# Kernel tuning notes

Hardware: AMD Instinct MI355X
Metric: run time of the kernel (lower is better)

The kernel has to match this reference:

```python
import jax, jax.numpy as jnp
import numpy as np

B, T, S, D, V = 8, 128, 256, 512, 32000
NEG_INF = -1e9


def setup_inputs() -> dict:
    key = jax.random.key(0)
    ks = jax.random.split(key, 10)
    sc = 1.0 / np.sqrt(D)
    return {
        "logits": jax.random.normal(ks[0], (B, T, D), jnp.float32),
        "encoded_text": jax.random.normal(ks[1], (B, S, D), jnp.float32),
        "encoded_tgt": jax.random.normal(ks[2], (B, T, D), jnp.float32),
        "text": jax.random.randint(ks[3], (B, S), 0, V),
        "text_mask": jnp.ones((B, 1, S), dtype=bool),
        "vocab_gen": jax.random.normal(ks[4], (V, D), jnp.float32) * sc,
        "Wq": jax.random.normal(ks[5], (D, D), jnp.float32) * sc,
        "bq": jnp.zeros((D,), jnp.float32),
        "Wk": jax.random.normal(ks[6], (D, D), jnp.float32) * sc,
        "bk": jnp.zeros((D,), jnp.float32),
        "Wp": jax.random.normal(ks[7], (1, 3 * D), jnp.float32) * sc,
        "bp": jnp.zeros((1,), jnp.float32),
    }


def reference(logits, encoded_text, encoded_tgt, text, text_mask,
              vocab_gen, Wq, bq, Wk, bk, Wp, bp):
    # vocab distribution: [B,T,V]
    vocab_attn = jnp.einsum('btd,vd->btv', logits, vocab_gen)
    p_vocab = jax.nn.softmax(vocab_attn, axis=-1)

    # single-head pointer attention (Annotated-Transformer style, h=1)
    q = logits @ Wq.T + bq            # [B,T,D]
    k = encoded_text @ Wk.T + bk      # [B,S,D]
    scores = jnp.einsum('btd,bsd->bts', q, k) / jnp.sqrt(jnp.float32(D))
    scores = jnp.where(text_mask, scores, NEG_INF)   # mask [B,1,S] broadcasts over T
    pointer_attn = jax.nn.softmax(scores, axis=-1)   # [B,T,S]

    # copy distribution via scatter-add over vocab dim
    b_idx = jnp.arange(B)[:, None, None]
    t_idx = jnp.arange(T)[None, :, None]
    text_index = jnp.broadcast_to(text[:, None, :], (B, T, S))
    p_text_ptr = jnp.zeros((B, T, V), p_vocab.dtype).at[b_idx, t_idx, text_index].add(pointer_attn)

    # attention-weighted context (original uses expand+repeat+sum; this is the same math)
    text_vec = jnp.einsum('bts,bsd->btd', pointer_attn, encoded_text)

    p_gen_vec = jnp.concatenate([logits, text_vec, encoded_tgt], axis=-1)  # [B,T,3D]
    switches = jax.nn.sigmoid(p_gen_vec @ Wp.T + bp)  # [B,T,1]

    p_out = (1.0 - switches) * p_text_ptr + switches * p_vocab
    return jnp.log(p_out)
```

## Files before the change

kernel.cpp:

```cpp
#include <hip/hip_runtime.h>

#define B_ 8
#define T_ 128
#define S_ 256
#define D_ 512
#define V_ 32000
#define BT_ 1024

typedef __attribute__((ext_vector_type(4))) float f32x4;
typedef __bf16 bf16x8 __attribute__((ext_vector_type(8)));

__device__ __forceinline__ unsigned short f2bf(float x) {
  union { float f; unsigned u; } c; c.f = x;
  unsigned r = c.u + 0x7fffu + ((c.u >> 16) & 1u);
  return (unsigned short)(r >> 16);
}
__device__ __forceinline__ float bf2f(unsigned short u) {
  union { unsigned u; float f; } c; c.u = ((unsigned)u) << 16;
  return c.f;
}

__global__ __launch_bounds__(256) void pg_cast_all(
    const float* __restrict__ logits, const float* __restrict__ vocab,
    const float* __restrict__ Wq, const float* __restrict__ Wk,
    const float* __restrict__ enc,
    unsigned short* __restrict__ Ab, unsigned short* __restrict__ Vgb,
    unsigned short* __restrict__ Wqb, unsigned short* __restrict__ Wkb,
    unsigned short* __restrict__ Etb) {
  int blk = blockIdx.x, tid = threadIdx.x;
  const float* in; unsigned short* out; int i;
  if (blk < 512)        { in = logits; out = Ab;  i = blk * 256 + tid; }
  else if (blk < 16512) { in = vocab;  out = Vgb; i = (blk - 512) * 256 + tid; }
  else if (blk < 16768) { in = Wq;     out = Wqb; i = (blk - 16512) * 256 + tid; }
  else if (blk < 17024) { in = Wk;     out = Wkb; i = (blk - 16768) * 256 + tid; }
  else                  { in = enc;    out = Etb; i = (blk - 17024) * 256 + tid; }
  float4 v = ((const float4*)in)[i];
  ushort4 o;
  o.x = f2bf(v.x); o.y = f2bf(v.y); o.z = f2bf(v.z); o.w = f2bf(v.w);
  ((ushort4*)out)[i] = o;
}

__global__ __launch_bounds__(256, 2) void pg_gemm_qk(
    const unsigned short* __restrict__ Ab, const unsigned short* __restrict__ Wqb,
    const unsigned short* __restrict__ Etb, const unsigned short* __restrict__ Wkb,
    float* __restrict__ qb, float* __restrict__ kb,
    const float* __restrict__ bq, const float* __restrict__ bk) {
  __shared__ unsigned short lds[2][2][128 * 64];
  int flat = blockIdx.x;
  const unsigned short *A, *Bm;
  float *C; const float* bias;
  int bx, by;
  if (flat < 32) {
    A = Ab; Bm = Wqb; C = qb; bias = bq;
    bx = flat & 3; by = flat >> 2;
  } else {
    int f = flat - 32;
    A = Etb; Bm = Wkb; C = kb; bias = bk;
    bx = f & 3; by = f >> 2;
  }
  const int K = 512;
  const int tid = threadIdx.x;
  const int w = tid >> 6, l = tid & 63;
  const int rowA0 = by * 128, rowB0 = bx * 128;
  const int wr = w >> 1, wc = w & 1;
  const int lr = l >> 3;
  const int cbl = (l & 7) * 16;

  f32x4 acc[4][4] = {};

  auto stage = [&](int buf, int kElem) {
#pragma unroll
    for (int i = 0; i < 4; ++i) {
      int chunk = i * 4 + w;
      int r = chunk * 8 + lr;
      int cByte = cbl ^ ((r & 7) << 4);
      const unsigned short* gA = A + (size_t)(rowA0 + r) * K + kElem + (cByte >> 1);
      __builtin_amdgcn_global_load_lds(
          (const __attribute__((address_space(1))) void*)gA,
          (__attribute__((address_space(3))) void*)&lds[buf][0][chunk * 512], 16, 0, 0);
      const unsigned short* gB = Bm + (size_t)(rowB0 + r) * K + kElem + (cByte >> 1);
      __builtin_amdgcn_global_load_lds(
          (const __attribute__((address_space(1))) void*)gB,
          (__attribute__((address_space(3))) void*)&lds[buf][1][chunk * 512], 16, 0, 0);
    }
  };

  const int fr = l & 15, fq = l >> 4;
  auto compute = [&](int buf) {
#pragma unroll
    for (int kk = 0; kk < 2; ++kk) {
      bf16x8 af[4], bff[4];
#pragma unroll
      for (int m = 0; m < 4; ++m) {
        int r = wr * 64 + m * 16 + fr;
        int cB = (kk * 64 + fq * 16) ^ ((r & 7) << 4);
        af[m] = *(const bf16x8*)((const char*)&lds[buf][0][0] + r * 128 + cB);
      }
#pragma unroll
      for (int n = 0; n < 4; ++n) {
        int r = wc * 64 + n * 16 + fr;
        int cB = (kk * 64 + fq * 16) ^ ((r & 7) << 4);
        bff[n] = *(const bf16x8*)((const char*)&lds[buf][1][0] + r * 128 + cB);
      }
#pragma unroll
      for (int m = 0; m < 4; ++m)
#pragma unroll
        for (int n = 0; n < 4; ++n)
          acc[m][n] = __builtin_amdgcn_mfma_f32_16x16x32_bf16(af[m], bff[n], acc[m][n], 0, 0, 0);
    }
  };

  stage(0, 0);
  __syncthreads();
  int buf = 0;
#pragma unroll
  for (int t = 0; t < 8; ++t) {
    if (t + 1 < 8) stage(buf ^ 1, (t + 1) << 6);
    compute(buf);
    __syncthreads();
    buf ^= 1;
  }

#pragma unroll
  for (int m = 0; m < 4; ++m) {
    int row = rowA0 + wr * 64 + m * 16 + fq * 4;
#pragma unroll
    for (int n = 0; n < 4; ++n) {
      int col = rowB0 + wc * 64 + n * 16 + fr;
      float bv = bias[col];
#pragma unroll
      for (int r = 0; r < 4; ++r)
        C[(size_t)(row + r) * 512 + col] = acc[m][n][r] + bv;
    }
  }
}

__global__ __launch_bounds__(256, 4) void pg_gemm_va(
    const unsigned short* __restrict__ A, const unsigned short* __restrict__ Bm,
    unsigned short* __restrict__ vab, float* __restrict__ pstats, int nbx) {
  __shared__ unsigned short lds[2][2][128 * 32];
  __shared__ float srow[128][2][2];
  const int K = 512;
  const int tid = threadIdx.x;
  const int w = tid >> 6, l = tid & 63;
  const int by = blockIdx.x;
  const int bx = blockIdx.y;
  const int rowA0 = by * 128, rowB0 = bx * 128;
  const int wr = w >> 1, wc = w & 1;
  const int lr = l >> 2;
  const int cbl = (l & 3) * 16;

  f32x4 acc[4][4] = {};

  auto stage = [&](int buf, int kElem) {
#pragma unroll
    for (int i = 0; i < 2; ++i) {
      int r = i * 64 + w * 16 + lr;
      int cByte = cbl ^ (((r >> 1) & 3) << 4);
      const unsigned short* gA = A + (size_t)(rowA0 + r) * K + kElem + (cByte >> 1);
      __builtin_amdgcn_global_load_lds(
          (const __attribute__((address_space(1))) void*)gA,
          (__attribute__((address_space(3))) void*)&lds[buf][0][i * 2048 + w * 512], 16, 0, 0);
      const unsigned short* gB = Bm + (size_t)(rowB0 + r) * K + kElem + (cByte >> 1);
      __builtin_amdgcn_global_load_lds(
          (const __attribute__((address_space(1))) void*)gB,
          (__attribute__((address_space(3))) void*)&lds[buf][1][i * 2048 + w * 512], 16, 0, 0);
    }
  };

  const int fr = l & 15, fq = l >> 4;
  auto compute = [&](int buf) {
    bf16x8 af[4], bff[4];
#pragma unroll
    for (int m = 0; m < 4; ++m) {
      int r = wr * 64 + m * 16 + fr;
      int cB = (fq * 16) ^ (((r >> 1) & 3) << 4);
      af[m] = *(const bf16x8*)((const char*)&lds[buf][0][0] + r * 64 + cB);
    }
#pragma unroll
    for (int n = 0; n < 4; ++n) {
      int r = wc * 64 + n * 16 + fr;
      int cB = (fq * 16) ^ (((r >> 1) & 3) << 4);
      bff[n] = *(const bf16x8*)((const char*)&lds[buf][1][0] + r * 64 + cB);
    }
#pragma unroll
    for (int m = 0; m < 4; ++m)
#pragma unroll
      for (int n = 0; n < 4; ++n)
        acc[m][n] = __builtin_amdgcn_mfma_f32_16x16x32_bf16(af[m], bff[n], acc[m][n], 0, 0, 0);
  };

  stage(0, 0);
  __syncthreads();
  int buf = 0;
#pragma unroll
  for (int t = 0; t < 16; ++t) {
    if (t + 1 < 16) stage(buf ^ 1, (t + 1) * 32);
    compute(buf);
    __syncthreads();
    buf ^= 1;
  }

#pragma unroll
  for (int m = 0; m < 4; ++m) {
    int row = rowA0 + wr * 64 + m * 16 + fq * 4;
#pragma unroll
    for (int n = 0; n < 4; ++n) {
      int col = rowB0 + wc * 64 + n * 16 + fr;
#pragma unroll
      for (int r = 0; r < 4; ++r) {
        float v = acc[m][n][r];
        float vn = __shfl_xor(v, 1);
        if ((l & 1) == 0) {
          unsigned pk = ((unsigned)f2bf(vn) << 16) | (unsigned)f2bf(v);
          *(unsigned*)(vab + (size_t)(row + r) * V_ + col) = pk;
        }
      }
    }
  }

#pragma unroll
  for (int m = 0; m < 4; ++m) {
#pragma unroll
    for (int r = 0; r < 4; ++r) {
      float mx = acc[m][0][r];
#pragma unroll
      for (int n = 1; n < 4; ++n) mx = fmaxf(mx, acc[m][n][r]);
      float sm = 0.f;
#pragma unroll
      for (int n = 0; n < 4; ++n) sm += __expf(acc[m][n][r] - mx);
#pragma unroll
      for (int off = 1; off < 16; off <<= 1) {
        float mx2 = __shfl_xor(mx, off);
        float sm2 = __shfl_xor(sm, off);
        float Mx = fmaxf(mx, mx2);
        sm = sm * __expf(mx - Mx) + sm2 * __expf(mx2 - Mx);
        mx = Mx;
      }
      if (fr == 0) {
        int rl = wr * 64 + m * 16 + fq * 4 + r;
        srow[rl][wc][0] = mx;
        srow[rl][wc][1] = sm;
      }
    }
  }
  __syncthreads();
  if (tid < 128) {
    float m0 = srow[tid][0][0], s0 = srow[tid][0][1];
    float m1 = srow[tid][1][0], s1 = srow[tid][1][1];
    float Mx = fmaxf(m0, m1);
    float S = s0 * __expf(m0 - Mx) + s1 * __expf(m1 - Mx);
    size_t idx = ((size_t)(rowA0 + tid) * nbx + bx) * 2;
    pstats[idx] = Mx;
    pstats[idx + 1] = S;
  }
}

__global__ __launch_bounds__(256) void pg_transpose_k(const float* __restrict__ in,
                                                      float* __restrict__ out) {
  __shared__ float tile[32][33];
  int dt = blockIdx.x * 32;
  int rt = blockIdx.y * 32;
  int tx = threadIdx.x, ty = threadIdx.y;
#pragma unroll
  for (int i = 0; i < 32; i += 8)
    tile[ty + i][tx] = in[(size_t)(rt + ty + i) * 512 + dt + tx];
  __syncthreads();
  int b = rt >> 8, s0 = rt & 255;
#pragma unroll
  for (int i = 0; i < 32; i += 8) {
    int d = dt + ty + i, s = s0 + tx;
    out[((size_t)b << 17) + ((size_t)d << 8) + s] = tile[tx][ty + i];
  }
}

__global__ __launch_bounds__(256) void pg_attn_tv(const float* __restrict__ q,
                                                  const float* __restrict__ kt,
                                                  const float* __restrict__ enc,
                                                  float* __restrict__ attn,
                                                  float* __restrict__ tv) {
  __shared__ float qsh[4][512];
  __shared__ float ash[4][256];
  __shared__ float red[2][4][4];
  int b = blockIdx.y, tg = blockIdx.x;
  int tid = threadIdx.x, w = tid >> 6, l = tid & 63;
  int row0 = b * T_ + tg * 4;
  for (int i = tid; i < 4 * 512; i += 256)
    qsh[i >> 9][i & 511] = q[(size_t)row0 * 512 + i] * 0.04419417382415922f;
  __syncthreads();
  float a0 = 0, a1 = 0, a2 = 0, a3 = 0;
  const float* kp = kt + ((size_t)b << 17) + tid;
  for (int d = 0; d < 512; ++d) {
    float kv = kp[(size_t)d << 8];
    a0 = fmaf(qsh[0][d], kv, a0);
    a1 = fmaf(qsh[1][d], kv, a1);
    a2 = fmaf(qsh[2][d], kv, a2);
    a3 = fmaf(qsh[3][d], kv, a3);
  }
  float acc[4] = {a0, a1, a2, a3};
#pragma unroll
  for (int j = 0; j < 4; ++j) {
    float m = acc[j];
    for (int off = 32; off; off >>= 1) m = fmaxf(m, __shfl_xor(m, off));
    if (l == 0) red[0][j][w] = m;
  }
  __syncthreads();
#pragma unroll
  for (int j = 0; j < 4; ++j) {
    float m = fmaxf(fmaxf(red[0][j][0], red[0][j][1]), fmaxf(red[0][j][2], red[0][j][3]));
    float e = __expf(acc[j] - m);
    acc[j] = e;
    float s = e;
    for (int off = 32; off; off >>= 1) s += __shfl_xor(s, off);
    if (l == 0) red[1][j][w] = s;
  }
  __syncthreads();
#pragma unroll
  for (int j = 0; j < 4; ++j) {
    float Z = red[1][j][0] + red[1][j][1] + red[1][j][2] + red[1][j][3];
    float p = acc[j] / Z;
    ash[j][tid] = p;
    attn[(size_t)(row0 + j) * 256 + tid] = p;
  }
  __syncthreads();
  float acc2[4][2] = {};
  const float* ep = enc + ((size_t)b << 17);
  for (int s = 0; s < 256; ++s) {
    float e0 = ep[(size_t)s * 512 + tid];
    float e1 = ep[(size_t)s * 512 + tid + 256];
#pragma unroll
    for (int j = 0; j < 4; ++j) {
      acc2[j][0] = fmaf(ash[j][s], e0, acc2[j][0]);
      acc2[j][1] = fmaf(ash[j][s], e1, acc2[j][1]);
    }
  }
#pragma unroll
  for (int j = 0; j < 4; ++j) {
    tv[(size_t)(row0 + j) * 512 + tid] = acc2[j][0];
    tv[(size_t)(row0 + j) * 512 + tid + 256] = acc2[j][1];
  }
}

__global__ __launch_bounds__(256) void pg_finalize(
    const unsigned short* __restrict__ vab, const float* __restrict__ pstat, int nbx,
    const float* __restrict__ attn, const int* __restrict__ text,
    const float* __restrict__ logits, const float* __restrict__ tvb,
    const float* __restrict__ tgt, const float* __restrict__ Wp,
    const float* __restrict__ bp, float* __restrict__ out) {
  __shared__ float redm[4], reds[4], redsw[4];
  __shared__ int tsh[256];
  __shared__ float ash[256];
  __shared__ float bcast[3];
  int bt = blockIdx.x, tid = threadIdx.x, w = tid >> 6, l = tid & 63;
  int b = bt >> 7;

  float m = -3.4e38f, s = 0.f;
  for (int j = tid; j < nbx; j += 256) {
    float2 p = ((const float2*)pstat)[(size_t)bt * nbx + j];
    float Mx = fmaxf(m, p.x);
    s = s * __expf(m - Mx) + p.y * __expf(p.x - Mx);
    m = Mx;
  }
  for (int off = 32; off; off >>= 1) {
    float m2 = __shfl_xor(m, off), s2 = __shfl_xor(s, off);
    float Mx = fmaxf(m, m2);
    s = s * __expf(m - Mx) + s2 * __expf(m2 - Mx);
    m = Mx;
  }
  if (l == 0) { redm[w] = m; reds[w] = s; }

  float a = 0;
  for (int j = tid; j < 512; j += 256) {
    a = fmaf(logits[(size_t)bt * 512 + j], Wp[j], a);
    a = fmaf(tvb[(size_t)bt * 512 + j], Wp[512 + j], a);
    a = fmaf(tgt[(size_t)bt * 512 + j], Wp[1024 + j], a);
  }
  for (int off = 32; off; off >>= 1) a += __shfl_xor(a, off);
  if (l == 0) redsw[w] = a;

  tsh[tid] = text[b * 256 + tid];
  ash[tid] = attn[(size_t)bt * 256 + tid];
  __syncthreads();
  if (tid == 0) {
    float M = fmaxf(fmaxf(redm[0], redm[1]), fmaxf(redm[2], redm[3]));
    float Z = reds[0] * __expf(redm[0] - M) + reds[1] * __expf(redm[1] - M) +
              reds[2] * __expf(redm[2] - M) + reds[3] * __expf(redm[3] - M);
    float t = redsw[0] + redsw[1] + redsw[2] + redsw[3] + bp[0];
    bcast[0] = M; bcast[1] = Z;
    bcast[2] = 1.f / (1.f + __expf(-t));
  }
  __syncthreads();
  float M = bcast[0], Z = bcast[1], swv = bcast[2];
  float cr = logf(swv) - M - logf(Z);

  const uint4* src = (const uint4*)(vab + (size_t)bt * V_);
  float4* dst = (float4*)(out + (size_t)bt * V_);
  for (int i = tid; i < 4000; i += 256) {
    uint4 u = src[i];
    float4 x, y;
    x.x = bf2f((unsigned short)(u.x & 0xffff)) + cr;
    x.y = bf2f((unsigned short)(u.x >> 16)) + cr;
    x.z = bf2f((unsigned short)(u.y & 0xffff)) + cr;
    x.w = bf2f((unsigned short)(u.y >> 16)) + cr;
    y.x = bf2f((unsigned short)(u.z & 0xffff)) + cr;
    y.y = bf2f((unsigned short)(u.z >> 16)) + cr;
    y.z = bf2f((unsigned short)(u.w & 0xffff)) + cr;
    y.w = bf2f((unsigned short)(u.w >> 16)) + cr;
    dst[i * 2] = x;
    dst[i * 2 + 1] = y;
  }

  int v = tsh[tid];
  bool first = true;
  float tot = 0.f;
  for (int s2 = 0; s2 < 256; ++s2) {
    if (tsh[s2] == v) {
      if (s2 < tid) first = false;
      tot += ash[s2];
    }
  }
  float pv = __expf(bf2f(vab[(size_t)bt * V_ + v]) - M) / Z;
  float val = logf(swv * pv + (1.f - swv) * tot);
  asm volatile("s_waitcnt vmcnt(0)" ::: "memory");
  __syncthreads();
  if (first)
    out[(size_t)bt * V_ + v] = val;
}

extern "C" void kernel_launch(void* const* d_in, const int* in_sizes, int n_in,
                              void* d_out, int out_size, void* d_ws, size_t ws_size,
                              hipStream_t stream) {
  const float* logits   = (const float*)d_in[0];
  const float* enc_text = (const float*)d_in[1];
  const float* enc_tgt  = (const float*)d_in[2];
  const int*   text     = (const int*)d_in[3];
  const float* vocab_gen = (const float*)d_in[5];
  const float* Wq = (const float*)d_in[6];
  const float* bq = (const float*)d_in[7];
  const float* Wk = (const float*)d_in[8];
  const float* bk = (const float*)d_in[9];
  const float* Wp = (const float*)d_in[10];
  const float* bp = (const float*)d_in[11];
  float* out = (float*)d_out;
  char* ws = (char*)d_ws;

  unsigned short* Ab  = (unsigned short*)(ws + 0);
  unsigned short* Vgb = (unsigned short*)(ws + 1048576);
  unsigned short* Wqb = (unsigned short*)(ws + 33816576);
  unsigned short* Wkb = (unsigned short*)(ws + 34340864);
  unsigned short* Etb = (unsigned short*)(ws + 34865152);
  float* qb    = (float*)(ws + 36962304);
  float* kb    = (float*)(ws + 39059456);
  float* ktb   = (float*)(ws + 43253760);
  float* attn  = (float*)(ws + 47448064);
  float* tvb   = (float*)(ws + 48496640);
  float* pstat = (float*)(ws + 51654656);
  unsigned short* vab = (unsigned short*)(ws + 53702656);

  pg_cast_all<<<dim3(18048), 256, 0, stream>>>(logits, vocab_gen, Wq, Wk, enc_text,
                                               Ab, Vgb, Wqb, Wkb, Etb);

  pg_gemm_qk<<<dim3(96), 256, 0, stream>>>(Ab, Wqb, Etb, Wkb, qb, kb, bq, bk);
  pg_transpose_k<<<dim3(16, 64), dim3(32, 8), 0, stream>>>(kb, ktb);
  pg_attn_tv<<<dim3(32, 8), 256, 0, stream>>>(qb, ktb, enc_text, attn, tvb);

  pg_gemm_va<<<dim3(8, 250), 256, 0, stream>>>(Ab, Vgb, vab, pstat, 250);

  pg_finalize<<<dim3(1024), 256, 0, stream>>>(vab, pstat, 250, attn, text,
                                              logits, tvb, enc_tgt, Wp, bp, out);
}
```

Before: 195.7 us.

## Merge Q/K projection GEMMs into vocab GEMM launch and write K transposed directly

The Q and K projection GEMMs now run inside the same launch as the large vocab-logit GEMM, dispatched by flat block index, so the small GEMMs share the grid with the big one instead of running as separate underfilled launches. The K epilogue writes its result already transposed as float4 stores, which removes the separate transpose kernel and the intermediate K buffer. The small GEMMs now use the vocab kernel's smaller 32-wide K tiles and 4-blocks-per-CU bounds, and blocks of different modes may be unevenly balanced.

```diff
diff --git a/kernel.cpp b/kernel.cpp
--- a/kernel.cpp
+++ b/kernel.cpp
@@ -40,111 +40,32 @@
   ((ushort4*)out)[i] = o;
 }
 
-__global__ __launch_bounds__(256, 2) void pg_gemm_qk(
-    const unsigned short* __restrict__ Ab, const unsigned short* __restrict__ Wqb,
-    const unsigned short* __restrict__ Etb, const unsigned short* __restrict__ Wkb,
-    float* __restrict__ qb, float* __restrict__ kb,
+__global__ __launch_bounds__(256, 4) void pg_gemm_big(
+    const unsigned short* __restrict__ Ab, const unsigned short* __restrict__ Vgb,
+    const unsigned short* __restrict__ Wqb, const unsigned short* __restrict__ Wkb,
+    const unsigned short* __restrict__ Etb,
+    unsigned short* __restrict__ vab, float* __restrict__ pstats, int nbx,
+    float* __restrict__ qb, float* __restrict__ ktb,
     const float* __restrict__ bq, const float* __restrict__ bk) {
-  __shared__ unsigned short lds[2][2][128 * 64];
-  int flat = blockIdx.x;
-  const unsigned short *A, *Bm;
-  float *C; const float* bias;
-  int bx, by;
-  if (flat < 32) {
-    A = Ab; Bm = Wqb; C = qb; bias = bq;
-    bx = flat & 3; by = flat >> 2;
-  } else {
-    int f = flat - 32;
-    A = Etb; Bm = Wkb; C = kb; bias = bk;
-    bx = f & 3; by = f >> 2;
-  }
-  const int K = 512;
-  const int tid = threadIdx.x;
-  const int w = tid >> 6, l = tid & 63;
-  const int rowA0 = by * 128, rowB0 = bx * 128;
-  const int wr = w >> 1, wc = w & 1;
-  const int lr = l >> 3;
-  const int cbl = (l & 7) * 16;
-
-  f32x4 acc[4][4] = {};
-
-  auto stage = [&](int buf, int kElem) {
-#pragma unroll
-    for (int i = 0; i < 4; ++i) {
-      int chunk = i * 4 + w;
-      int r = chunk * 8 + lr;
-      int cByte = cbl ^ ((r & 7) << 4);
-      const unsigned short* gA = A + (size_t)(rowA0 + r) * K + kElem + (cByte >> 1);
-      __builtin_amdgcn_global_load_lds(
-          (const __attribute__((address_space(1))) void*)gA,
-          (__attribute__((address_space(3))) void*)&lds[buf][0][chunk * 512], 16, 0, 0);
-      const unsigned short* gB = Bm + (size_t)(rowB0 + r) * K + kElem + (cByte >> 1);
-      __builtin_amdgcn_global_load_lds(
-          (const __attribute__((address_space(1))) void*)gB,
-          (__attribute__((address_space(3))) void*)&lds[buf][1][chunk * 512], 16, 0, 0);
-    }
-  };
-
-  const int fr = l & 15, fq = l >> 4;
-  auto compute = [&](int buf) {
-#pragma unroll
-    for (int kk = 0; kk < 2; ++kk) {
-      bf16x8 af[4], bff[4];
-#pragma unroll
-      for (int m = 0; m < 4; ++m) {
-        int r = wr * 64 + m * 16 + fr;
-        int cB = (kk * 64 + fq * 16) ^ ((r & 7) << 4);
-        af[m] = *(const bf16x8*)((const char*)&lds[buf][0][0] + r * 128 + cB);
-      }
-#pragma unroll
-      for (int n = 0; n < 4; ++n) {
-        int r = wc * 64 + n * 16 + fr;
-        int cB = (kk * 64 + fq * 16) ^ ((r & 7) << 4);
-        bff[n] = *(const bf16x8*)((const char*)&lds[buf][1][0] + r * 128 + cB);
-      }
-#pragma unroll
-      for (int m = 0; m < 4; ++m)
-#pragma unroll
-        for (int n = 0; n < 4; ++n)
-          acc[m][n] = __builtin_amdgcn_mfma_f32_16x16x32_bf16(af[m], bff[n], acc[m][n], 0, 0, 0);
-    }
-  };
-
-  stage(0, 0);
-  __syncthreads();
-  int buf = 0;
-#pragma unroll
-  for (int t = 0; t < 8; ++t) {
-    if (t + 1 < 8) stage(buf ^ 1, (t + 1) << 6);
-    compute(buf);
-    __syncthreads();
-    buf ^= 1;
-  }
-
-#pragma unroll
-  for (int m = 0; m < 4; ++m) {
-    int row = rowA0 + wr * 64 + m * 16 + fq * 4;
-#pragma unroll
-    for (int n = 0; n < 4; ++n) {
-      int col = rowB0 + wc * 64 + n * 16 + fr;
-      float bv = bias[col];
-#pragma unroll
-      for (int r = 0; r < 4; ++r)
-        C[(size_t)(row + r) * 512 + col] = acc[m][n][r] + bv;
-    }
-  }
-}
-
-__global__ __launch_bounds__(256, 4) void pg_gemm_va(
-    const unsigned short* __restrict__ A, const unsigned short* __restrict__ Bm,
-    unsigned short* __restrict__ vab, float* __restrict__ pstats, int nbx) {
   __shared__ unsigned short lds[2][2][128 * 32];
   __shared__ float srow[128][2][2];
   const int K = 512;
+  const int flat = blockIdx.x;
   const int tid = threadIdx.x;
   const int w = tid >> 6, l = tid & 63;
-  const int by = blockIdx.x;
-  const int bx = blockIdx.y;
+
+  const unsigned short *A, *Bm;
+  int bx, by, mode;
+  if (flat < 2000) {
+    mode = 0; by = flat & 7; bx = flat >> 3;
+    A = Ab; Bm = Vgb;
+  } else if (flat < 2032) {
+    mode = 1; int f = flat - 2000; bx = f & 3; by = f >> 2;
+    A = Ab; Bm = Wqb;
+  } else {
+    mode = 2; int f = flat - 2032; bx = f & 3; by = f >> 2;
+    A = Etb; Bm = Wkb;
+  }
   const int rowA0 = by * 128, rowB0 = bx * 128;
   const int wr = w >> 1, wc = w & 1;
   const int lr = l >> 2;
@@ -199,6 +120,39 @@
     compute(buf);
     __syncthreads();
     buf ^= 1;
+  }
+
+  if (mode == 1) {
+#pragma unroll
+    for (int m = 0; m < 4; ++m) {
+      int row = rowA0 + wr * 64 + m * 16 + fq * 4;
+#pragma unroll
+      for (int n = 0; n < 4; ++n) {
+        int col = rowB0 + wc * 64 + n * 16 + fr;
+        float bv = bq[col];
+#pragma unroll
+        for (int r = 0; r < 4; ++r)
+          qb[(size_t)(row + r) * 512 + col] = acc[m][n][r] + bv;
+      }
+    }
+    return;
+  }
+  if (mode == 2) {
+    int b = rowA0 >> 8;
+#pragma unroll
+    for (int m = 0; m < 4; ++m) {
+      int row = rowA0 + wr * 64 + m * 16 + fq * 4;
+      int s0 = row & 255;
+#pragma unroll
+      for (int n = 0; n < 4; ++n) {
+        int col = rowB0 + wc * 64 + n * 16 + fr;
+        float bv = bk[col];
+        float4 v = {acc[m][n][0] + bv, acc[m][n][1] + bv,
+                    acc[m][n][2] + bv, acc[m][n][3] + bv};
+        *(float4*)(ktb + ((size_t)b << 17) + ((size_t)col << 8) + s0) = v;
+      }
+    }
+    return;
   }
 
 #pragma unroll
@@ -253,24 +207,6 @@
     size_t idx = ((size_t)(rowA0 + tid) * nbx + bx) * 2;
     pstats[idx] = Mx;
     pstats[idx + 1] = S;
-  }
-}
-
-__global__ __launch_bounds__(256) void pg_transpose_k(const float* __restrict__ in,
-                                                      float* __restrict__ out) {
-  __shared__ float tile[32][33];
-  int dt = blockIdx.x * 32;
-  int rt = blockIdx.y * 32;
-  int tx = threadIdx.x, ty = threadIdx.y;
-#pragma unroll
-  for (int i = 0; i < 32; i += 8)
-    tile[ty + i][tx] = in[(size_t)(rt + ty + i) * 512 + dt + tx];
-  __syncthreads();
-  int b = rt >> 8, s0 = rt & 255;
-#pragma unroll
-  for (int i = 0; i < 32; i += 8) {
-    int d = dt + ty + i, s = s0 + tx;
-    out[((size_t)b << 17) + ((size_t)d << 8) + s] = tile[tx][ty + i];
   }
 }
 
@@ -450,7 +386,6 @@
   unsigned short* Wkb = (unsigned short*)(ws + 34340864);
   unsigned short* Etb = (unsigned short*)(ws + 34865152);
   float* qb    = (float*)(ws + 36962304);
-  float* kb    = (float*)(ws + 39059456);
   float* ktb   = (float*)(ws + 43253760);
   float* attn  = (float*)(ws + 47448064);
   float* tvb   = (float*)(ws + 48496640);
@@ -460,11 +395,10 @@
   pg_cast_all<<<dim3(18048), 256, 0, stream>>>(logits, vocab_gen, Wq, Wk, enc_text,
                                                Ab, Vgb, Wqb, Wkb, Etb);
 
-  pg_gemm_qk<<<dim3(96), 256, 0, stream>>>(Ab, Wqb, Etb, Wkb, qb, kb, bq, bk);
-  pg_transpose_k<<<dim3(16, 64), dim3(32, 8), 0, stream>>>(kb, ktb);
+  pg_gemm_big<<<dim3(2096), 256, 0, stream>>>(Ab, Vgb, Wqb, Wkb, Etb,
+                                              vab, pstat, 250, qb, ktb, bq, bk);
+
   pg_attn_tv<<<dim3(32, 8), 256, 0, stream>>>(qb, ktb, enc_text, attn, tvb);
-
-  pg_gemm_va<<<dim3(8, 250), 256, 0, stream>>>(Ab, Vgb, vab, pstat, 250);
 
   pg_finalize<<<dim3(1024), 256, 0, stream>>>(vab, pstat, 250, attn, text,
                                               logits, tvb, enc_tgt, Wp, bp, out);
```

Result: faster. 181.5 us (-7.2%).
